# Kernel optimization log

Hardware: AMD Instinct MI355X
Metric: run time of the kernel (lower is better)

## Reference

```python
import jax, jax.numpy as jnp
import numpy as np

H, N, S, R, CH, LMAX = 512, 32, 1, 1, 1, 1024


def _to_c(x):
    # torch.view_as_real storage -> complex
    return x[..., 0] + 1j * x[..., 1]


def _rep(x, v):
    # einops: '... t n -> ... (v t) n'  (tile trainable copies up to H)
    shp = x.shape
    x = jnp.broadcast_to(x[..., None, :, :], shp[:-2] + (v,) + shp[-2:])
    return x.reshape(shp[:-2] + (v * shp[-2], shp[-1]))


def setup_inputs() -> dict:
    key = jax.random.key(0)
    k1, k2, k3, k4, k5 = jax.random.split(key, 5)
    # dt log-uniform in [1e-3, 1e-1] (S4 default init)
    log_dt = jax.random.uniform(k1, (H,), jnp.float32,
                                minval=float(np.log(1e-3)), maxval=float(np.log(1e-1)))
    # real_type='exp': w_real = -exp(inv_w_real); init around -0.5
    inv_w_real = jnp.log(0.5) * jnp.ones((S, N), jnp.float32) \
        + 0.1 * jax.random.normal(k2, (S, N), jnp.float32)
    w_imag = jnp.broadcast_to(jnp.pi * jnp.arange(N, dtype=jnp.float32), (S, N))
    B_ri = jax.random.normal(k3, (1, S, N, 2), jnp.float32)
    C_ri = jax.random.normal(k4, (CH, H, N, 2), jnp.float32)
    P_ri = 0.5 * jax.random.normal(k5, (R, S, N, 2), jnp.float32)
    return {"log_dt": log_dt, "inv_w_real": inv_w_real, "w_imag": w_imag,
            "B_ri": B_ri, "C_ri": C_ri, "P_ri": P_ri, "L": LMAX}


def _kernel(log_dt, inv_w_real, w_imag, B_ri, C_ri, P_ri, L):
    dt = jnp.exp(log_dt)                                    # (H,)
    w = -jnp.exp(inv_w_real) + 1j * w_imag                  # (S, N), real_type='exp'
    B = _to_c(B_ri)                                         # (1, S, N)
    C = _to_c(C_ri)                                         # (c, H, N)
    P = _to_c(P_ri)                                         # (R, S, N)
    Q = jnp.conj(P)
    v_rep = log_dt.shape[0] // w.shape[0]                   # broadcast = H // S
    B, P, Q = _rep(B, v_rep), _rep(P, v_rep), _rep(Q, v_rep)
    w = _rep(w, v_rep)                                      # (H, N)
    rank = P.shape[0]

    # FFT nodes and bilinear-transformed nodes
    Lf = L // 2 + 1
    omega = jnp.exp(-2j * jnp.pi * jnp.arange(Lf) / L).astype(jnp.complex64)
    z = 2 * (1 - omega) / (1 + omega)                       # (Lf,)

    # Stack B with P and C with Q for batched Cauchy
    Bst = jnp.concatenate([B, P], axis=-3)                  # (1+R, H, N)
    Cst = jnp.concatenate([C, Q], axis=-3)                  # (c+R, H, N)
    v = Bst[:, None] * Cst[None]                            # (1+R, c+R, H, N)
    w_dt = w * dt[:, None]                                  # (H, N): dt folded into A

    # Cauchy kernel with conjugate-pair extension: sum_n v/(z-w) + conj(v)/(z-conj(w))
    v2 = jnp.concatenate([v, jnp.conj(v)], axis=-1)         # (1+R, c+R, H, 2N)
    w2 = jnp.concatenate([w_dt, jnp.conj(w_dt)], axis=-1)   # (H, 2N)
    r = jnp.sum(v2[..., None] / (z - w2[..., :, None]), axis=-2)  # (1+R, c+R, H, Lf)
    r = r * dt[None, None, :, None]

    # Woodbury correction for the low-rank part
    r00 = r[:-rank, :-rank]                                 # (1, c, H, Lf)
    r01 = r[:-rank, -rank:]                                 # (1, R, H, Lf)
    r10 = r[-rank:, :-rank]                                 # (R, c, H, Lf)
    r11 = r[-rank:, -rank:]                                 # (R, R, H, Lf)
    r11 = jnp.moveaxis(r11, (0, 1), (-2, -1))               # (H, Lf, R, R)
    r11 = jnp.linalg.inv(jnp.eye(rank, dtype=r.dtype) + r11)
    r11 = jnp.moveaxis(r11, (-2, -1), (0, 1))               # (R, R, H, Lf)
    k_f = r00 - jnp.einsum('ijhl,jkhl,kmhl->imhl', r01, r11, r10)

    # Undo bilinear transform and go to time domain
    k_f = k_f * 2 / (1 + omega)
    k = jnp.fft.irfft(k_f, n=L, axis=-1)[..., :L]           # (1, c, H, L) real
    return k[-1]                                            # k_B: (c, H, L)


def reference(log_dt, inv_w_real, w_imag, B_ri, C_ri, P_ri, L):
    return _kernel(log_dt, inv_w_real, w_imag, B_ri, C_ri, P_ri, L)
```

## Files before the change

### kernel.cpp

```cpp
#include <hip/hip_runtime.h>
#include <math.h>

#define H_DIM 512
#define N_DIM 32
#define L_LEN 1024

typedef float v2f __attribute__((ext_vector_type(2)));
__device__ __forceinline__ v2f splat2(float a) { return (v2f){a, a}; }


__launch_bounds__(576, 5)
__global__ void ssk_nplr_kernel(const float* __restrict__ log_dt,
                                const float* __restrict__ inv_w_real,
                                const float* __restrict__ w_imag,
                                const float* __restrict__ B_ri,
                                const float* __restrict__ C_ri,
                                const float* __restrict__ P_ri,
                                float* __restrict__ out)
{
    __shared__ float2 Ksh[513];
    __shared__ float2 polD[N_DIM];
    __shared__ float4 polA[N_DIM];
    __shared__ float4 polB[N_DIM];
    __shared__ float  Sre[512], Sim[512];

    const int t = threadIdx.x;
    const int h = blockIdx.x;
    const float dt = expf(log_dt[h]);

    if (t < N_DIM) {
        const int n = t;
        float wr = -expf(inv_w_real[n]);
        float wi = w_imag[n];
        float wdx = wr * dt, wdy = wi * dt;
        float Bx = B_ri[2*n],               By = B_ri[2*n+1];
        float Cx = C_ri[h*2*N_DIM + 2*n],   Cy = C_ri[h*2*N_DIM + 2*n+1];
        float Px = P_ri[2*n],               Py = P_ri[2*n+1];
        float v00x = Bx*Cx - By*Cy, v00y = Bx*Cy + By*Cx;
        float v01x = Bx*Px + By*Py, v01y = By*Px - Bx*Py;
        float v10x = Px*Cx - Py*Cy, v10y = Px*Cy + Py*Cx;
        float v11x = Px*Px + Py*Py;
        polD[n] = make_float2(-2.0f*wdx, wdx*wdx + wdy*wdy);
        polA[n] = make_float4(2.0f*v00x, 2.0f*v01x, 2.0f*v10x, 2.0f*v11x);
        polB[n] = make_float4(2.0f*(v00x*wdx + v00y*wdy),
                              2.0f*(v01x*wdx + v01y*wdy),
                              2.0f*(v10x*wdx + v10y*wdy),
                              2.0f*(v11x*wdx));
    }

    float w256c, w256s, w128c, w128s, w64c, w64s;
    float w32c, w32s, w16c, w16s, w8c, w8s, w4c, w4s;
    {
        float r256 = (float)(t & 255) * (1.0f/512.0f);
        float r128 = (float)(t & 127) * (1.0f/256.0f);
        float r64  = (float)(t &  63) * (1.0f/128.0f);
        float r32  = (float)(t &  31) * (1.0f/64.0f);
        float r16  = (float)(t &  15) * (1.0f/32.0f);
        float r8   = (float)(t &   7) * (1.0f/16.0f);
        float r4   = (float)(t &   3) * (1.0f/8.0f);
        w256s = __builtin_amdgcn_sinf(r256); w256c = __builtin_amdgcn_cosf(r256);
        w128s = __builtin_amdgcn_sinf(r128); w128c = __builtin_amdgcn_cosf(r128);
        w64s  = __builtin_amdgcn_sinf(r64);  w64c  = __builtin_amdgcn_cosf(r64);
        w32s  = __builtin_amdgcn_sinf(r32);  w32c  = __builtin_amdgcn_cosf(r32);
        w16s  = __builtin_amdgcn_sinf(r16);  w16c  = __builtin_amdgcn_cosf(r16);
        w8s   = __builtin_amdgcn_sinf(r8);   w8c   = __builtin_amdgcn_cosf(r8);
        w4s   = __builtin_amdgcn_sinf(r4);   w4c   = __builtin_amdgcn_cosf(r4);
    }

    const int j = (t < 512) ? t : 512;
    float si, co;
    if (j == 512) {
        si = 8.7422777e-8f;
        co = -1.0f;
    } else {
        float rev = (float)j * (-0.0009765625f);
        si = __builtin_amdgcn_sinf(rev);
        co = __builtin_amdgcn_cosf(rev);
    }
    __syncthreads();

    float px = 1.0f + co, py = si;
    float pinv = 1.0f / (px*px + py*py);
    float ipx = px*pinv, ipy = -py*pinv;
    float mx = 1.0f - co, my = -si;
    float zx = 2.0f*(mx*ipx - my*ipy);
    float zy = 2.0f*(mx*ipy + my*ipx);

    v2f Z  = { zx, zy };
    v2f Z2 = { zx*zx - zy*zy, 2.0f*zx*zy };

    v2f U0{0,0}, U1{0,0}, U2{0,0}, U3{0,0};
    v2f V0{0,0}, V1{0,0}, V2{0,0}, V3{0,0};
    #pragma unroll 4
    for (int n = 0; n < N_DIM; ++n) {
        float2 d  = polD[n];
        float4 A  = polA[n];
        float4 Bv = polB[n];
        v2f D = __builtin_elementwise_fma(splat2(d.x), Z, Z2);
        D.x += d.y;
        float s  = __builtin_amdgcn_rcpf(fmaf(D.x, D.x, D.y*D.y));
        v2f R = { D.x * s, -(D.y * s) };
        U0 = __builtin_elementwise_fma(splat2(A.x),  R, U0);
        U1 = __builtin_elementwise_fma(splat2(A.y),  R, U1);
        U2 = __builtin_elementwise_fma(splat2(A.z),  R, U2);
        U3 = __builtin_elementwise_fma(splat2(A.w),  R, U3);
        V0 = __builtin_elementwise_fma(splat2(Bv.x), R, V0);
        V1 = __builtin_elementwise_fma(splat2(Bv.y), R, V1);
        V2 = __builtin_elementwise_fma(splat2(Bv.z), R, V2);
        V3 = __builtin_elementwise_fma(splat2(Bv.w), R, V3);
    }
    float r00x = dt*(zx*U0.x - zy*U0.y - V0.x), r00y = dt*(zx*U0.y + zy*U0.x - V0.y);
    float r01x = dt*(zx*U1.x - zy*U1.y - V1.x), r01y = dt*(zx*U1.y + zy*U1.x - V1.y);
    float r10x = dt*(zx*U2.x - zy*U2.y - V2.x), r10y = dt*(zx*U2.y + zy*U2.x - V2.y);
    float r11x = dt*(zx*U3.x - zy*U3.y - V3.x), r11y = dt*(zx*U3.y + zy*U3.x - V3.y);

    float dnx = 1.0f + r11x, dny = r11y;
    float dinv = 1.0f / (dnx*dnx + dny*dny);
    float idx_ = dnx*dinv, idy = -dny*dinv;
    float m01x = r01x*r10x - r01y*r10y;
    float m01y = r01x*r10y + r01y*r10x;
    float kfx = r00x - (m01x*idx_ - m01y*idy);
    float kfy = r00y - (m01x*idy + m01y*idx_);
    float fxv = 2.0f*(kfx*ipx - kfy*ipy);
    float fyv = 2.0f*(kfx*ipy + kfy*ipx);
    if (t <= 512) Ksh[j] = make_float2(fxv, fyv);
    __syncthreads();

    float xr = 0.0f, xi = 0.0f;
    if (t < 512) {
        float2 Ka = Ksh[t];
        float2 Kb = Ksh[512 - t];
        const int tb = t ^ 256;
        float2 Kc = Ksh[tb];
        float2 Kd = Ksh[512 - tb];
        float Wx = co, Wy = -si;
        float hsx = 0.5f*(Ka.x + Kb.x), hsy = 0.5f*(Ka.y - Kb.y);
        float hdx = 0.5f*(Ka.x - Kb.x), hdy = 0.5f*(Ka.y + Kb.y);
        float Yax = hsx - Wy*hdx - Wx*hdy;
        float Yay = hsy - Wy*hdy + Wx*hdx;
        float Wbx = (t < 256) ? -Wy :  Wy;
        float Wby = (t < 256) ?  Wx : -Wx;
        float hsx2 = 0.5f*(Kc.x + Kd.x), hsy2 = 0.5f*(Kc.y - Kd.y);
        float hdx2 = 0.5f*(Kc.x - Kd.x), hdy2 = 0.5f*(Kc.y + Kd.y);
        float Ybx = hsx2 - Wby*hdx2 - Wbx*hdy2;
        float Yby = hsy2 - Wby*hdy2 + Wbx*hdx2;
        if (t & 256) {
            float dr = Ybx - Yax, di = Yby - Yay;
            xr = dr*w256c - di*w256s; xi = dr*w256s + di*w256c;
        } else {
            xr = Yax + Ybx; xi = Yay + Yby;
        }
        Sre[t] = xr; Sim[t] = xi;
    }
    __syncthreads();

    if (t < 512) {
        {
            float p1r = Sre[t ^ 128], p1i = Sim[t ^ 128];
            float p2r = Sre[t ^  64], p2i = Sim[t ^  64];
            float p3r = Sre[t ^ 192], p3i = Sim[t ^ 192];
            float Atr, Ati, Apr, Api;
            if (t & 128) {
                float dr = p1r - xr, di = p1i - xi;
                Atr = dr*w128c - di*w128s; Ati = dr*w128s + di*w128c;
                float er = p3r - p2r, ei = p3i - p2i;
                float wpr = (t & 64) ?  w128s : -w128s;
                float wpi = (t & 64) ? -w128c :  w128c;
                Apr = er*wpr - ei*wpi; Api = er*wpi + ei*wpr;
            } else {
                Atr = xr + p1r;  Ati = xi + p1i;
                Apr = p2r + p3r; Api = p2i + p3i;
            }
            if (t & 64) {
                float dr = Apr - Atr, di = Api - Ati;
                xr = dr*w64c - di*w64s; xi = dr*w64s + di*w64c;
            } else { xr = Atr + Apr; xi = Ati + Api; }
        }

        #define RADIX4S(S_, W1C, W1S, W2C, W2S) {                               \
            float p1r = __shfl_xor(xr, S_),        p1i = __shfl_xor(xi, S_);    \
            float p2r = __shfl_xor(xr, S_/2),      p2i = __shfl_xor(xi, S_/2);  \
            float p3r = __shfl_xor(xr, S_ + S_/2), p3i = __shfl_xor(xi, S_ + S_/2); \
            float Atr, Ati, Apr, Api;                                           \
            if (t & S_) {                                                       \
                float dr = p1r - xr, di = p1i - xi;                             \
                Atr = dr*W1C - di*W1S; Ati = dr*W1S + di*W1C;                   \
                float er = p3r - p2r, ei = p3i - p2i;                           \
                float wpr = (t & (S_/2)) ?  W1S : -W1S;                         \
                float wpi = (t & (S_/2)) ? -W1C :  W1C;                         \
                Apr = er*wpr - ei*wpi; Api = er*wpi + ei*wpr;                   \
            } else {                                                            \
                Atr = xr + p1r;  Ati = xi + p1i;                                \
                Apr = p2r + p3r; Api = p2i + p3i;                               \
            }                                                                   \
            if (t & (S_/2)) {                                                   \
                float dr = Apr - Atr, di = Api - Ati;                           \
                xr = dr*W2C - di*W2S; xi = dr*W2S + di*W2C;                     \
            } else { xr = Atr + Apr; xi = Ati + Api; }                          \
        }
        RADIX4S(32, w32c, w32s, w16c, w16s)
        RADIX4S(8,  w8c,  w8s,  w4c,  w4s)
        #undef RADIX4S

        {
            float p1r = __shfl_xor(xr, 2), p1i = __shfl_xor(xi, 2);
            float p2r = __shfl_xor(xr, 1), p2i = __shfl_xor(xi, 1);
            float p3r = __shfl_xor(xr, 3), p3i = __shfl_xor(xi, 3);
            float Atr, Ati, Apr, Api;
            if (t & 2) {
                float dr = p1r - xr, di = p1i - xi;
                float er = p3r - p2r, ei = p3i - p2i;
                if (t & 1) { Atr = -di; Ati =  dr;
                             Apr =  er; Api =  ei; }
                else       { Atr =  dr; Ati =  di;
                             Apr = -ei; Api =  er; }
            } else {
                Atr = xr + p1r;  Ati = xi + p1i;
                Apr = p2r + p3r; Api = p2i + p3i;
            }
            if (t & 1) { xr = Apr - Atr; xi = Api - Ati; }
            else       { xr = Atr + Apr; xi = Ati + Api; }
        }

        unsigned m = __brev((unsigned)t) >> 23;
        ((float2*)out)[h*512 + m] = make_float2(xr*(1.0f/512.0f), xi*(1.0f/512.0f));
    }
}

extern "C" void kernel_launch(void* const* d_in, const int* in_sizes, int n_in,
                              void* d_out, int out_size, void* d_ws, size_t ws_size,
                              hipStream_t stream) {
    const float* log_dt     = (const float*)d_in[0];
    const float* inv_w_real = (const float*)d_in[1];
    const float* w_imag     = (const float*)d_in[2];
    const float* B_ri       = (const float*)d_in[3];
    const float* C_ri       = (const float*)d_in[4];
    const float* P_ri       = (const float*)d_in[5];

    ssk_nplr_kernel<<<H_DIM, 576, 0, stream>>>(log_dt, inv_w_real, w_imag,
                                               B_ri, C_ri, P_ri, (float*)d_out);
}
```

Before: 15.86 us.

## Split Cauchy evaluation and inverse FFT into two kernels with N-split reduction

Splits the fused kernel into a Cauchy kernel and an iFFT kernel that exchange the frequency response through a workspace buffer. The Cauchy kernel uses a 2D grid over frequency chunks, splits the 32-term sum across four thread groups and reduces their partials through shared memory. This is meant to raise parallelism and shorten each thread's serial loop. In exchange it adds a second launch, a global round trip for kf, and wastes most of the last frequency block (only j=512 is valid there).

```diff
diff --git a/kernel.cpp b/kernel.cpp
--- a/kernel.cpp
+++ b/kernel.cpp
@@ -4,28 +4,31 @@
 #define H_DIM 512
 #define N_DIM 32
 #define L_LEN 1024
+#define LF 513
 
 typedef float v2f __attribute__((ext_vector_type(2)));
-__device__ __forceinline__ v2f splat2(float a) { return (v2f){a, a}; }
-
-
-__launch_bounds__(576, 5)
-__global__ void ssk_nplr_kernel(const float* __restrict__ log_dt,
-                                const float* __restrict__ inv_w_real,
-                                const float* __restrict__ w_imag,
-                                const float* __restrict__ B_ri,
-                                const float* __restrict__ C_ri,
-                                const float* __restrict__ P_ri,
-                                float* __restrict__ out)
+static __device__ __forceinline__ v2f splat2(float a) { return (v2f){a, a}; }
+
+__launch_bounds__(512, 8)
+__global__ void k1_cauchy(const float* __restrict__ log_dt,
+                          const float* __restrict__ inv_w_real,
+                          const float* __restrict__ w_imag,
+                          const float* __restrict__ B_ri,
+                          const float* __restrict__ C_ri,
+                          const float* __restrict__ P_ri,
+                          float2* __restrict__ kf)
 {
-    __shared__ float2 Ksh[513];
     __shared__ float2 polD[N_DIM];
     __shared__ float4 polA[N_DIM];
     __shared__ float4 polB[N_DIM];
-    __shared__ float  Sre[512], Sim[512];
-
-    const int t = threadIdx.x;
-    const int h = blockIdx.x;
+    __shared__ float4 comb[4][4][128];
+
+    const int t  = threadIdx.x;
+    const int h  = blockIdx.x;
+    const int jl = t & 127;
+    const int ph = t >> 7;
+    const int j  = blockIdx.y * 128 + jl;
+    const bool active = (j <= 512);
     const float dt = expf(log_dt[h]);
 
     if (t < N_DIM) {
@@ -47,27 +50,8 @@
                               2.0f*(v10x*wdx + v10y*wdy),
                               2.0f*(v11x*wdx));
     }
-
-    float w256c, w256s, w128c, w128s, w64c, w64s;
-    float w32c, w32s, w16c, w16s, w8c, w8s, w4c, w4s;
-    {
-        float r256 = (float)(t & 255) * (1.0f/512.0f);
-        float r128 = (float)(t & 127) * (1.0f/256.0f);
-        float r64  = (float)(t &  63) * (1.0f/128.0f);
-        float r32  = (float)(t &  31) * (1.0f/64.0f);
-        float r16  = (float)(t &  15) * (1.0f/32.0f);
-        float r8   = (float)(t &   7) * (1.0f/16.0f);
-        float r4   = (float)(t &   3) * (1.0f/8.0f);
-        w256s = __builtin_amdgcn_sinf(r256); w256c = __builtin_amdgcn_cosf(r256);
-        w128s = __builtin_amdgcn_sinf(r128); w128c = __builtin_amdgcn_cosf(r128);
-        w64s  = __builtin_amdgcn_sinf(r64);  w64c  = __builtin_amdgcn_cosf(r64);
-        w32s  = __builtin_amdgcn_sinf(r32);  w32c  = __builtin_amdgcn_cosf(r32);
-        w16s  = __builtin_amdgcn_sinf(r16);  w16c  = __builtin_amdgcn_cosf(r16);
-        w8s   = __builtin_amdgcn_sinf(r8);   w8c   = __builtin_amdgcn_cosf(r8);
-        w4s   = __builtin_amdgcn_sinf(r4);   w4c   = __builtin_amdgcn_cosf(r4);
-    }
-
-    const int j = (t < 512) ? t : 512;
+    __syncthreads();
+
     float si, co;
     if (j == 512) {
         si = 8.7422777e-8f;
@@ -77,7 +61,6 @@
         si = __builtin_amdgcn_sinf(rev);
         co = __builtin_amdgcn_cosf(rev);
     }
-    __syncthreads();
 
     float px = 1.0f + co, py = si;
     float pinv = 1.0f / (px*px + py*py);
@@ -91,8 +74,10 @@
 
     v2f U0{0,0}, U1{0,0}, U2{0,0}, U3{0,0};
     v2f V0{0,0}, V1{0,0}, V2{0,0}, V3{0,0};
-    #pragma unroll 4
-    for (int n = 0; n < N_DIM; ++n) {
+    const int n0 = ph * 8;
+    #pragma unroll
+    for (int k = 0; k < 8; ++k) {
+        const int n = n0 + k;
         float2 d  = polD[n];
         float4 A  = polA[n];
         float4 Bv = polB[n];
@@ -109,25 +94,81 @@
         V2 = __builtin_elementwise_fma(splat2(Bv.z), R, V2);
         V3 = __builtin_elementwise_fma(splat2(Bv.w), R, V3);
     }
-    float r00x = dt*(zx*U0.x - zy*U0.y - V0.x), r00y = dt*(zx*U0.y + zy*U0.x - V0.y);
-    float r01x = dt*(zx*U1.x - zy*U1.y - V1.x), r01y = dt*(zx*U1.y + zy*U1.x - V1.y);
-    float r10x = dt*(zx*U2.x - zy*U2.y - V2.x), r10y = dt*(zx*U2.y + zy*U2.x - V2.y);
-    float r11x = dt*(zx*U3.x - zy*U3.y - V3.x), r11y = dt*(zx*U3.y + zy*U3.x - V3.y);
-
-    float dnx = 1.0f + r11x, dny = r11y;
-    float dinv = 1.0f / (dnx*dnx + dny*dny);
-    float idx_ = dnx*dinv, idy = -dny*dinv;
-    float m01x = r01x*r10x - r01y*r10y;
-    float m01y = r01x*r10y + r01y*r10x;
-    float kfx = r00x - (m01x*idx_ - m01y*idy);
-    float kfy = r00y - (m01x*idy + m01y*idx_);
-    float fxv = 2.0f*(kfx*ipx - kfy*ipy);
-    float fyv = 2.0f*(kfx*ipy + kfy*ipx);
-    if (t <= 512) Ksh[j] = make_float2(fxv, fyv);
-    __syncthreads();
-
-    float xr = 0.0f, xi = 0.0f;
-    if (t < 512) {
+
+    comb[ph][0][jl] = make_float4(U0.x, U0.y, U1.x, U1.y);
+    comb[ph][1][jl] = make_float4(U2.x, U2.y, U3.x, U3.y);
+    comb[ph][2][jl] = make_float4(V0.x, V0.y, V1.x, V1.y);
+    comb[ph][3][jl] = make_float4(V2.x, V2.y, V3.x, V3.y);
+    __syncthreads();
+
+    if (ph == 0 && active) {
+        #pragma unroll
+        for (int p = 1; p < 4; ++p) {
+            float4 c0 = comb[p][0][jl];
+            float4 c1 = comb[p][1][jl];
+            float4 c2 = comb[p][2][jl];
+            float4 c3 = comb[p][3][jl];
+            U0.x += c0.x; U0.y += c0.y; U1.x += c0.z; U1.y += c0.w;
+            U2.x += c1.x; U2.y += c1.y; U3.x += c1.z; U3.y += c1.w;
+            V0.x += c2.x; V0.y += c2.y; V1.x += c2.z; V1.y += c2.w;
+            V2.x += c3.x; V2.y += c3.y; V3.x += c3.z; V3.y += c3.w;
+        }
+        float r00x = dt*(zx*U0.x - zy*U0.y - V0.x), r00y = dt*(zx*U0.y + zy*U0.x - V0.y);
+        float r01x = dt*(zx*U1.x - zy*U1.y - V1.x), r01y = dt*(zx*U1.y + zy*U1.x - V1.y);
+        float r10x = dt*(zx*U2.x - zy*U2.y - V2.x), r10y = dt*(zx*U2.y + zy*U2.x - V2.y);
+        float r11x = dt*(zx*U3.x - zy*U3.y - V3.x), r11y = dt*(zx*U3.y + zy*U3.x - V3.y);
+
+        float dnx = 1.0f + r11x, dny = r11y;
+        float dinv = 1.0f / (dnx*dnx + dny*dny);
+        float idx_ = dnx*dinv, idy = -dny*dinv;
+        float m01x = r01x*r10x - r01y*r10y;
+        float m01y = r01x*r10y + r01y*r10x;
+        float kfx = r00x - (m01x*idx_ - m01y*idy);
+        float kfy = r00y - (m01x*idy + m01y*idx_);
+        float fxv = 2.0f*(kfx*ipx - kfy*ipy);
+        float fyv = 2.0f*(kfx*ipy + kfy*ipx);
+        kf[h*LF + j] = make_float2(fxv, fyv);
+    }
+}
+
+__launch_bounds__(512, 8)
+__global__ void k2_ifft(const float2* __restrict__ kf,
+                        float* __restrict__ out)
+{
+    __shared__ float2 Ksh[LF];
+    __shared__ float  Sre[512], Sim[512];
+
+    const int t = threadIdx.x;
+    const int h = blockIdx.x;
+
+    Ksh[t] = kf[h*LF + t];
+    if (t == 0) Ksh[512] = kf[h*LF + 512];
+
+    float w256c, w256s, w128c, w128s, w64c, w64s;
+    float w32c, w32s, w16c, w16s, w8c, w8s, w4c, w4s;
+    {
+        float r256 = (float)(t & 255) * (1.0f/512.0f);
+        float r128 = (float)(t & 127) * (1.0f/256.0f);
+        float r64  = (float)(t &  63) * (1.0f/128.0f);
+        float r32  = (float)(t &  31) * (1.0f/64.0f);
+        float r16  = (float)(t &  15) * (1.0f/32.0f);
+        float r8   = (float)(t &   7) * (1.0f/16.0f);
+        float r4   = (float)(t &   3) * (1.0f/8.0f);
+        w256s = __builtin_amdgcn_sinf(r256); w256c = __builtin_amdgcn_cosf(r256);
+        w128s = __builtin_amdgcn_sinf(r128); w128c = __builtin_amdgcn_cosf(r128);
+        w64s  = __builtin_amdgcn_sinf(r64);  w64c  = __builtin_amdgcn_cosf(r64);
+        w32s  = __builtin_amdgcn_sinf(r32);  w32c  = __builtin_amdgcn_cosf(r32);
+        w16s  = __builtin_amdgcn_sinf(r16);  w16c  = __builtin_amdgcn_cosf(r16);
+        w8s   = __builtin_amdgcn_sinf(r8);   w8c   = __builtin_amdgcn_cosf(r8);
+        w4s   = __builtin_amdgcn_sinf(r4);   w4c   = __builtin_amdgcn_cosf(r4);
+    }
+    float rev = (float)t * (-0.0009765625f);
+    float si = __builtin_amdgcn_sinf(rev);
+    float co = __builtin_amdgcn_cosf(rev);
+    __syncthreads();
+
+    float xr, xi;
+    {
         float2 Ka = Ksh[t];
         float2 Kb = Ksh[512 - t];
         const int tb = t ^ 256;
@@ -154,77 +195,75 @@
     }
     __syncthreads();
 
-    if (t < 512) {
-        {
-            float p1r = Sre[t ^ 128], p1i = Sim[t ^ 128];
-            float p2r = Sre[t ^  64], p2i = Sim[t ^  64];
-            float p3r = Sre[t ^ 192], p3i = Sim[t ^ 192];
-            float Atr, Ati, Apr, Api;
-            if (t & 128) {
-                float dr = p1r - xr, di = p1i - xi;
-                Atr = dr*w128c - di*w128s; Ati = dr*w128s + di*w128c;
-                float er = p3r - p2r, ei = p3i - p2i;
-                float wpr = (t & 64) ?  w128s : -w128s;
-                float wpi = (t & 64) ? -w128c :  w128c;
-                Apr = er*wpr - ei*wpi; Api = er*wpi + ei*wpr;
-            } else {
-                Atr = xr + p1r;  Ati = xi + p1i;
-                Apr = p2r + p3r; Api = p2i + p3i;
-            }
-            if (t & 64) {
-                float dr = Apr - Atr, di = Api - Ati;
-                xr = dr*w64c - di*w64s; xi = dr*w64s + di*w64c;
-            } else { xr = Atr + Apr; xi = Ati + Api; }
-        }
-
-        #define RADIX4S(S_, W1C, W1S, W2C, W2S) {                               \
-            float p1r = __shfl_xor(xr, S_),        p1i = __shfl_xor(xi, S_);    \
-            float p2r = __shfl_xor(xr, S_/2),      p2i = __shfl_xor(xi, S_/2);  \
-            float p3r = __shfl_xor(xr, S_ + S_/2), p3i = __shfl_xor(xi, S_ + S_/2); \
-            float Atr, Ati, Apr, Api;                                           \
-            if (t & S_) {                                                       \
-                float dr = p1r - xr, di = p1i - xi;                             \
-                Atr = dr*W1C - di*W1S; Ati = dr*W1S + di*W1C;                   \
-                float er = p3r - p2r, ei = p3i - p2i;                           \
-                float wpr = (t & (S_/2)) ?  W1S : -W1S;                         \
-                float wpi = (t & (S_/2)) ? -W1C :  W1C;                         \
-                Apr = er*wpr - ei*wpi; Api = er*wpi + ei*wpr;                   \
-            } else {                                                            \
-                Atr = xr + p1r;  Ati = xi + p1i;                                \
-                Apr = p2r + p3r; Api = p2i + p3i;                               \
-            }                                                                   \
-            if (t & (S_/2)) {                                                   \
-                float dr = Apr - Atr, di = Api - Ati;                           \
-                xr = dr*W2C - di*W2S; xi = dr*W2S + di*W2C;                     \
-            } else { xr = Atr + Apr; xi = Ati + Api; }                          \
-        }
-        RADIX4S(32, w32c, w32s, w16c, w16s)
-        RADIX4S(8,  w8c,  w8s,  w4c,  w4s)
-        #undef RADIX4S
-
-        {
-            float p1r = __shfl_xor(xr, 2), p1i = __shfl_xor(xi, 2);
-            float p2r = __shfl_xor(xr, 1), p2i = __shfl_xor(xi, 1);
-            float p3r = __shfl_xor(xr, 3), p3i = __shfl_xor(xi, 3);
-            float Atr, Ati, Apr, Api;
-            if (t & 2) {
-                float dr = p1r - xr, di = p1i - xi;
-                float er = p3r - p2r, ei = p3i - p2i;
-                if (t & 1) { Atr = -di; Ati =  dr;
-                             Apr =  er; Api =  ei; }
-                else       { Atr =  dr; Ati =  di;
-                             Apr = -ei; Api =  er; }
-            } else {
-                Atr = xr + p1r;  Ati = xi + p1i;
-                Apr = p2r + p3r; Api = p2i + p3i;
-            }
-            if (t & 1) { xr = Apr - Atr; xi = Api - Ati; }
-            else       { xr = Atr + Apr; xi = Ati + Api; }
-        }
-
-        unsigned m = __brev((unsigned)t) >> 23;
-        ((float2*)out)[h*512 + m] = make_float2(xr*(1.0f/512.0f), xi*(1.0f/512.0f));
-    }
+    {
+        float p1r = Sre[t ^ 128], p1i = Sim[t ^ 128];
+        float p2r = Sre[t ^  64], p2i = Sim[t ^  64];
+        float p3r = Sre[t ^ 192], p3i = Sim[t ^ 192];
+        float Atr, Ati, Apr, Api;
+        if (t & 128) {
+            float dr = p1r - xr, di = p1i - xi;
+            Atr = dr*w128c - di*w128s; Ati = dr*w128s + di*w128c;
+            float er = p3r - p2r, ei = p3i - p2i;
+            float wpr = (t & 64) ?  w128s : -w128s;
+            float wpi = (t & 64) ? -w128c :  w128c;
+            Apr = er*wpr - ei*wpi; Api = er*wpi + ei*wpr;
+        } else {
+            Atr = xr + p1r;  Ati = xi + p1i;
+            Apr = p2r + p3r; Api = p2i + p3i;
+        }
+        if (t & 64) {
+            float dr = Apr - Atr, di = Api - Ati;
+            xr = dr*w64c - di*w64s; xi = dr*w64s + di*w64c;
+        } else { xr = Atr + Apr; xi = Ati + Api; }
+    }
+
+    #define RADIX4S(S_, W1C, W1S, W2C, W2S) {                               \
+        float p1r = __shfl_xor(xr, S_),        p1i = __shfl_xor(xi, S_);    \
+        float p2r = __shfl_xor(xr, S_/2),      p2i = __shfl_xor(xi, S_/2);  \
+        float p3r = __shfl_xor(xr, S_ + S_/2), p3i = __shfl_xor(xi, S_ + S_/2); \
+        float Atr, Ati, Apr, Api;                                           \
+        if (t & S_) {                                                       \
+            float dr = p1r - xr, di = p1i - xi;                             \
+            Atr = dr*W1C - di*W1S; Ati = dr*W1S + di*W1C;                   \
+            float er = p3r - p2r, ei = p3i - p2i;                           \
+            float wpr = (t & (S_/2)) ?  W1S : -W1S;                         \
+            float wpi = (t & (S_/2)) ? -W1C :  W1C;                         \
+            Apr = er*wpr - ei*wpi; Api = er*wpi + ei*wpr;                   \
+        } else {                                                            \
+            Atr = xr + p1r;  Ati = xi + p1i;                                \
+            Apr = p2r + p3r; Api = p2i + p3i;                               \
+        }                                                                   \
+        if (t & (S_/2)) {                                                   \
+            float dr = Apr - Atr, di = Api - Ati;                           \
+            xr = dr*W2C - di*W2S; xi = dr*W2S + di*W2C;                     \
+        } else { xr = Atr + Apr; xi = Ati + Api; }                          \
+    }
+    RADIX4S(32, w32c, w32s, w16c, w16s)
+    RADIX4S(8,  w8c,  w8s,  w4c,  w4s)
+    #undef RADIX4S
+
+    {
+        float p1r = __shfl_xor(xr, 2), p1i = __shfl_xor(xi, 2);
+        float p2r = __shfl_xor(xr, 1), p2i = __shfl_xor(xi, 1);
+        float p3r = __shfl_xor(xr, 3), p3i = __shfl_xor(xi, 3);
+        float Atr, Ati, Apr, Api;
+        if (t & 2) {
+            float dr = p1r - xr, di = p1i - xi;
+            float er = p3r - p2r, ei = p3i - p2i;
+            if (t & 1) { Atr = -di; Ati =  dr;
+                         Apr =  er; Api =  ei; }
+            else       { Atr =  dr; Ati =  di;
+                         Apr = -ei; Api =  er; }
+        } else {
+            Atr = xr + p1r;  Ati = xi + p1i;
+            Apr = p2r + p3r; Api = p2i + p3i;
+        }
+        if (t & 1) { xr = Apr - Atr; xi = Api - Ati; }
+        else       { xr = Atr + Apr; xi = Ati + Api; }
+    }
+
+    unsigned m = __brev((unsigned)t) >> 23;
+    ((float2*)out)[h*512 + m] = make_float2(xr*(1.0f/512.0f), xi*(1.0f/512.0f));
 }
 
 extern "C" void kernel_launch(void* const* d_in, const int* in_sizes, int n_in,
@@ -237,6 +276,10 @@
     const float* C_ri       = (const float*)d_in[4];
     const float* P_ri       = (const float*)d_in[5];
 
-    ssk_nplr_kernel<<<H_DIM, 576, 0, stream>>>(log_dt, inv_w_real, w_imag,
-                                               B_ri, C_ri, P_ri, (float*)d_out);
+    float2* kf = (float2*)d_ws;
+
+    dim3 g1(H_DIM, 5);
+    k1_cauchy<<<g1, 512, 0, stream>>>(log_dt, inv_w_real, w_imag,
+                                      B_ri, C_ri, P_ri, kf);
+    k2_ifft<<<H_DIM, 512, 0, stream>>>(kf, (float*)d_out);
 }
```

Result: slower. 19.35 us (+22.0%).

## Compute two frequency nodes per thread in Cauchy stage, shrink block to 512

Applied to the files above, without the earlier changes.

Block size drops from 576 to 512 threads. In the Cauchy/Woodbury stage, threads 0..256 now each evaluate two frequency nodes (j and j+256), so the shared-memory loads of the pole coefficients are reused across both nodes and the partial wavefront of 64 extra threads goes away. The FFT stage keeps one point per thread and its twiddle is computed separately. In exchange, about half the threads sit idle during the Cauchy loop, and register pressure rises from the doubled accumulators.

```diff
diff --git a/kernel.cpp b/kernel.cpp
--- a/kernel.cpp
+++ b/kernel.cpp
@@ -3,13 +3,31 @@
 
 #define H_DIM 512
 #define N_DIM 32
-#define L_LEN 1024
 
 typedef float v2f __attribute__((ext_vector_type(2)));
-__device__ __forceinline__ v2f splat2(float a) { return (v2f){a, a}; }
-
-
-__launch_bounds__(576, 5)
+static __device__ __forceinline__ v2f splat2(float a) { return (v2f){a, a}; }
+
+static __device__ __forceinline__ float2 woodbury(
+    v2f U0, v2f U1, v2f U2, v2f U3,
+    v2f V0, v2f V1, v2f V2, v2f V3,
+    float zx, float zy, float dt, float ipx, float ipy)
+{
+    float r00x = dt*(zx*U0.x - zy*U0.y - V0.x), r00y = dt*(zx*U0.y + zy*U0.x - V0.y);
+    float r01x = dt*(zx*U1.x - zy*U1.y - V1.x), r01y = dt*(zx*U1.y + zy*U1.x - V1.y);
+    float r10x = dt*(zx*U2.x - zy*U2.y - V2.x), r10y = dt*(zx*U2.y + zy*U2.x - V2.y);
+    float r11x = dt*(zx*U3.x - zy*U3.y - V3.x), r11y = dt*(zx*U3.y + zy*U3.x - V3.y);
+    float dnx = 1.0f + r11x, dny = r11y;
+    float dinv = 1.0f / (dnx*dnx + dny*dny);
+    float idx_ = dnx*dinv, idy = -dny*dinv;
+    float m01x = r01x*r10x - r01y*r10y;
+    float m01y = r01x*r10y + r01y*r10x;
+    float kfx = r00x - (m01x*idx_ - m01y*idy);
+    float kfy = r00y - (m01x*idy + m01y*idx_);
+    return make_float2(2.0f*(kfx*ipx - kfy*ipy),
+                       2.0f*(kfx*ipy + kfy*ipx));
+}
+
+__launch_bounds__(512, 4)
 __global__ void ssk_nplr_kernel(const float* __restrict__ log_dt,
                                 const float* __restrict__ inv_w_real,
                                 const float* __restrict__ w_imag,
@@ -66,74 +84,100 @@
         w8s   = __builtin_amdgcn_sinf(r8);   w8c   = __builtin_amdgcn_cosf(r8);
         w4s   = __builtin_amdgcn_sinf(r4);   w4c   = __builtin_amdgcn_cosf(r4);
     }
-
-    const int j = (t < 512) ? t : 512;
-    float si, co;
-    if (j == 512) {
-        si = 8.7422777e-8f;
-        co = -1.0f;
-    } else {
-        float rev = (float)j * (-0.0009765625f);
-        si = __builtin_amdgcn_sinf(rev);
-        co = __builtin_amdgcn_cosf(rev);
+    float Wx, Wy;
+    {
+        float pr = (float)t * 0.0009765625f;
+        Wy = __builtin_amdgcn_sinf(pr);
+        Wx = __builtin_amdgcn_cosf(pr);
     }
     __syncthreads();
 
-    float px = 1.0f + co, py = si;
-    float pinv = 1.0f / (px*px + py*py);
-    float ipx = px*pinv, ipy = -py*pinv;
-    float mx = 1.0f - co, my = -si;
-    float zx = 2.0f*(mx*ipx - my*ipy);
-    float zy = 2.0f*(mx*ipy + my*ipx);
-
-    v2f Z  = { zx, zy };
-    v2f Z2 = { zx*zx - zy*zy, 2.0f*zx*zy };
-
-    v2f U0{0,0}, U1{0,0}, U2{0,0}, U3{0,0};
-    v2f V0{0,0}, V1{0,0}, V2{0,0}, V3{0,0};
-    #pragma unroll 4
-    for (int n = 0; n < N_DIM; ++n) {
-        float2 d  = polD[n];
-        float4 A  = polA[n];
-        float4 Bv = polB[n];
-        v2f D = __builtin_elementwise_fma(splat2(d.x), Z, Z2);
-        D.x += d.y;
-        float s  = __builtin_amdgcn_rcpf(fmaf(D.x, D.x, D.y*D.y));
-        v2f R = { D.x * s, -(D.y * s) };
-        U0 = __builtin_elementwise_fma(splat2(A.x),  R, U0);
-        U1 = __builtin_elementwise_fma(splat2(A.y),  R, U1);
-        U2 = __builtin_elementwise_fma(splat2(A.z),  R, U2);
-        U3 = __builtin_elementwise_fma(splat2(A.w),  R, U3);
-        V0 = __builtin_elementwise_fma(splat2(Bv.x), R, V0);
-        V1 = __builtin_elementwise_fma(splat2(Bv.y), R, V1);
-        V2 = __builtin_elementwise_fma(splat2(Bv.z), R, V2);
-        V3 = __builtin_elementwise_fma(splat2(Bv.w), R, V3);
-    }
-    float r00x = dt*(zx*U0.x - zy*U0.y - V0.x), r00y = dt*(zx*U0.y + zy*U0.x - V0.y);
-    float r01x = dt*(zx*U1.x - zy*U1.y - V1.x), r01y = dt*(zx*U1.y + zy*U1.x - V1.y);
-    float r10x = dt*(zx*U2.x - zy*U2.y - V2.x), r10y = dt*(zx*U2.y + zy*U2.x - V2.y);
-    float r11x = dt*(zx*U3.x - zy*U3.y - V3.x), r11y = dt*(zx*U3.y + zy*U3.x - V3.y);
-
-    float dnx = 1.0f + r11x, dny = r11y;
-    float dinv = 1.0f / (dnx*dnx + dny*dny);
-    float idx_ = dnx*dinv, idy = -dny*dinv;
-    float m01x = r01x*r10x - r01y*r10y;
-    float m01y = r01x*r10y + r01y*r10x;
-    float kfx = r00x - (m01x*idx_ - m01y*idy);
-    float kfy = r00y - (m01x*idy + m01y*idx_);
-    float fxv = 2.0f*(kfx*ipx - kfy*ipy);
-    float fyv = 2.0f*(kfx*ipy + kfy*ipx);
-    if (t <= 512) Ksh[j] = make_float2(fxv, fyv);
+    if (t < 257) {
+        const int j1 = t, j2 = t + 256;
+        float s1, c1, s2, c2;
+        {
+            float rev1 = (float)j1 * (-0.0009765625f);
+            s1 = __builtin_amdgcn_sinf(rev1);
+            c1 = __builtin_amdgcn_cosf(rev1);
+        }
+        if (j2 == 512) {
+            s2 = 8.7422777e-8f;
+            c2 = -1.0f;
+        } else {
+            float rev2 = (float)j2 * (-0.0009765625f);
+            s2 = __builtin_amdgcn_sinf(rev2);
+            c2 = __builtin_amdgcn_cosf(rev2);
+        }
+
+        float pxa = 1.0f + c1, pya = s1;
+        float pia = 1.0f / (pxa*pxa + pya*pya);
+        float ipxa = pxa*pia, ipya = -pya*pia;
+        float mxa = 1.0f - c1, mya = -s1;
+        float zxa = 2.0f*(mxa*ipxa - mya*ipya);
+        float zya = 2.0f*(mxa*ipya + mya*ipxa);
+
+        float pxb = 1.0f + c2, pyb = s2;
+        float pib = 1.0f / (pxb*pxb + pyb*pyb);
+        float ipxb = pxb*pib, ipyb = -pyb*pib;
+        float mxb = 1.0f - c2, myb = -s2;
+        float zxb = 2.0f*(mxb*ipxb - myb*ipyb);
+        float zyb = 2.0f*(mxb*ipyb + myb*ipxb);
+
+        v2f Za  = { zxa, zya };
+        v2f Z2a = { zxa*zxa - zya*zya, 2.0f*zxa*zya };
+        v2f Zb  = { zxb, zyb };
+        v2f Z2b = { zxb*zxb - zyb*zyb, 2.0f*zxb*zyb };
+
+        v2f Ua0{0,0}, Ua1{0,0}, Ua2{0,0}, Ua3{0,0};
+        v2f Va0{0,0}, Va1{0,0}, Va2{0,0}, Va3{0,0};
+        v2f Ub0{0,0}, Ub1{0,0}, Ub2{0,0}, Ub3{0,0};
+        v2f Vb0{0,0}, Vb1{0,0}, Vb2{0,0}, Vb3{0,0};
+
+        #pragma unroll 4
+        for (int n = 0; n < N_DIM; ++n) {
+            float2 d  = polD[n];
+            float4 A  = polA[n];
+            float4 Bv = polB[n];
+            v2f Da = __builtin_elementwise_fma(splat2(d.x), Za, Z2a);
+            Da.x += d.y;
+            v2f Db = __builtin_elementwise_fma(splat2(d.x), Zb, Z2b);
+            Db.x += d.y;
+            float sa = __builtin_amdgcn_rcpf(fmaf(Da.x, Da.x, Da.y*Da.y));
+            float sb = __builtin_amdgcn_rcpf(fmaf(Db.x, Db.x, Db.y*Db.y));
+            v2f Ra = { Da.x * sa, -(Da.y * sa) };
+            v2f Rb = { Db.x * sb, -(Db.y * sb) };
+            Ua0 = __builtin_elementwise_fma(splat2(A.x),  Ra, Ua0);
+            Ua1 = __builtin_elementwise_fma(splat2(A.y),  Ra, Ua1);
+            Ua2 = __builtin_elementwise_fma(splat2(A.z),  Ra, Ua2);
+            Ua3 = __builtin_elementwise_fma(splat2(A.w),  Ra, Ua3);
+            Va0 = __builtin_elementwise_fma(splat2(Bv.x), Ra, Va0);
+            Va1 = __builtin_elementwise_fma(splat2(Bv.y), Ra, Va1);
+            Va2 = __builtin_elementwise_fma(splat2(Bv.z), Ra, Va2);
+            Va3 = __builtin_elementwise_fma(splat2(Bv.w), Ra, Va3);
+            Ub0 = __builtin_elementwise_fma(splat2(A.x),  Rb, Ub0);
+            Ub1 = __builtin_elementwise_fma(splat2(A.y),  Rb, Ub1);
+            Ub2 = __builtin_elementwise_fma(splat2(A.z),  Rb, Ub2);
+            Ub3 = __builtin_elementwise_fma(splat2(A.w),  Rb, Ub3);
+            Vb0 = __builtin_elementwise_fma(splat2(Bv.x), Rb, Vb0);
+            Vb1 = __builtin_elementwise_fma(splat2(Bv.y), Rb, Vb1);
+            Vb2 = __builtin_elementwise_fma(splat2(Bv.z), Rb, Vb2);
+            Vb3 = __builtin_elementwise_fma(splat2(Bv.w), Rb, Vb3);
+        }
+
+        Ksh[j1] = woodbury(Ua0, Ua1, Ua2, Ua3, Va0, Va1, Va2, Va3,
+                           zxa, zya, dt, ipxa, ipya);
+        Ksh[j2] = woodbury(Ub0, Ub1, Ub2, Ub3, Vb0, Vb1, Vb2, Vb3,
+                           zxb, zyb, dt, ipxb, ipyb);
+    }
     __syncthreads();
 
-    float xr = 0.0f, xi = 0.0f;
-    if (t < 512) {
+    float xr, xi;
+    {
         float2 Ka = Ksh[t];
         float2 Kb = Ksh[512 - t];
         const int tb = t ^ 256;
         float2 Kc = Ksh[tb];
         float2 Kd = Ksh[512 - tb];
-        float Wx = co, Wy = -si;
         float hsx = 0.5f*(Ka.x + Kb.x), hsy = 0.5f*(Ka.y - Kb.y);
         float hdx = 0.5f*(Ka.x - Kb.x), hdy = 0.5f*(Ka.y + Kb.y);
         float Yax = hsx - Wy*hdx - Wx*hdy;
@@ -154,77 +198,75 @@
     }
     __syncthreads();
 
-    if (t < 512) {
-        {
-            float p1r = Sre[t ^ 128], p1i = Sim[t ^ 128];
-            float p2r = Sre[t ^  64], p2i = Sim[t ^  64];
-            float p3r = Sre[t ^ 192], p3i = Sim[t ^ 192];
-            float Atr, Ati, Apr, Api;
-            if (t & 128) {
-                float dr = p1r - xr, di = p1i - xi;
-                Atr = dr*w128c - di*w128s; Ati = dr*w128s + di*w128c;
-                float er = p3r - p2r, ei = p3i - p2i;
-                float wpr = (t & 64) ?  w128s : -w128s;
-                float wpi = (t & 64) ? -w128c :  w128c;
-                Apr = er*wpr - ei*wpi; Api = er*wpi + ei*wpr;
-            } else {
-                Atr = xr + p1r;  Ati = xi + p1i;
-                Apr = p2r + p3r; Api = p2i + p3i;
-            }
-            if (t & 64) {
-                float dr = Apr - Atr, di = Api - Ati;
-                xr = dr*w64c - di*w64s; xi = dr*w64s + di*w64c;
-            } else { xr = Atr + Apr; xi = Ati + Api; }
-        }
-
-        #define RADIX4S(S_, W1C, W1S, W2C, W2S) {                               \
-            float p1r = __shfl_xor(xr, S_),        p1i = __shfl_xor(xi, S_);    \
-            float p2r = __shfl_xor(xr, S_/2),      p2i = __shfl_xor(xi, S_/2);  \
-            float p3r = __shfl_xor(xr, S_ + S_/2), p3i = __shfl_xor(xi, S_ + S_/2); \
-            float Atr, Ati, Apr, Api;                                           \
-            if (t & S_) {                                                       \
-                float dr = p1r - xr, di = p1i - xi;                             \
-                Atr = dr*W1C - di*W1S; Ati = dr*W1S + di*W1C;                   \
-                float er = p3r - p2r, ei = p3i - p2i;                           \
-                float wpr = (t & (S_/2)) ?  W1S : -W1S;                         \
-                float wpi = (t & (S_/2)) ? -W1C :  W1C;                         \
-                Apr = er*wpr - ei*wpi; Api = er*wpi + ei*wpr;                   \
-            } else {                                                            \
-                Atr = xr + p1r;  Ati = xi + p1i;                                \
-                Apr = p2r + p3r; Api = p2i + p3i;                               \
-            }                                                                   \
-            if (t & (S_/2)) {                                                   \
-                float dr = Apr - Atr, di = Api - Ati;                           \
-                xr = dr*W2C - di*W2S; xi = dr*W2S + di*W2C;                     \
-            } else { xr = Atr + Apr; xi = Ati + Api; }                          \
-        }
-        RADIX4S(32, w32c, w32s, w16c, w16s)
-        RADIX4S(8,  w8c,  w8s,  w4c,  w4s)
-        #undef RADIX4S
-
-        {
-            float p1r = __shfl_xor(xr, 2), p1i = __shfl_xor(xi, 2);
-            float p2r = __shfl_xor(xr, 1), p2i = __shfl_xor(xi, 1);
-            float p3r = __shfl_xor(xr, 3), p3i = __shfl_xor(xi, 3);
-            float Atr, Ati, Apr, Api;
-            if (t & 2) {
-                float dr = p1r - xr, di = p1i - xi;
-                float er = p3r - p2r, ei = p3i - p2i;
-                if (t & 1) { Atr = -di; Ati =  dr;
-                             Apr =  er; Api =  ei; }
-                else       { Atr =  dr; Ati =  di;
-                             Apr = -ei; Api =  er; }
-            } else {
-                Atr = xr + p1r;  Ati = xi + p1i;
-                Apr = p2r + p3r; Api = p2i + p3i;
-            }
-            if (t & 1) { xr = Apr - Atr; xi = Api - Ati; }
-            else       { xr = Atr + Apr; xi = Ati + Api; }
-        }
-
-        unsigned m = __brev((unsigned)t) >> 23;
-        ((float2*)out)[h*512 + m] = make_float2(xr*(1.0f/512.0f), xi*(1.0f/512.0f));
-    }
+    {
+        float p1r = Sre[t ^ 128], p1i = Sim[t ^ 128];
+        float p2r = Sre[t ^  64], p2i = Sim[t ^  64];
+        float p3r = Sre[t ^ 192], p3i = Sim[t ^ 192];
+        float Atr, Ati, Apr, Api;
+        if (t & 128) {
+            float dr = p1r - xr, di = p1i - xi;
+            Atr = dr*w128c - di*w128s; Ati = dr*w128s + di*w128c;
+            float er = p3r - p2r, ei = p3i - p2i;
+            float wpr = (t & 64) ?  w128s : -w128s;
+            float wpi = (t & 64) ? -w128c :  w128c;
+            Apr = er*wpr - ei*wpi; Api = er*wpi + ei*wpr;
+        } else {
+            Atr = xr + p1r;  Ati = xi + p1i;
+            Apr = p2r + p3r; Api = p2i + p3i;
+        }
+        if (t & 64) {
+            float dr = Apr - Atr, di = Api - Ati;
+            xr = dr*w64c - di*w64s; xi = dr*w64s + di*w64c;
+        } else { xr = Atr + Apr; xi = Ati + Api; }
+    }
+
+    #define RADIX4S(S_, W1C, W1S, W2C, W2S) {                               \
+        float p1r = __shfl_xor(xr, S_),        p1i = __shfl_xor(xi, S_);    \
+        float p2r = __shfl_xor(xr, S_/2),      p2i = __shfl_xor(xi, S_/2);  \
+        float p3r = __shfl_xor(xr, S_ + S_/2), p3i = __shfl_xor(xi, S_ + S_/2); \
+        float Atr, Ati, Apr, Api;                                           \
+        if (t & S_) {                                                       \
+            float dr = p1r - xr, di = p1i - xi;                             \
+            Atr = dr*W1C - di*W1S; Ati = dr*W1S + di*W1C;                   \
+            float er = p3r - p2r, ei = p3i - p2i;                           \
+            float wpr = (t & (S_/2)) ?  W1S : -W1S;                         \
+            float wpi = (t & (S_/2)) ? -W1C :  W1C;                         \
+            Apr = er*wpr - ei*wpi; Api = er*wpi + ei*wpr;                   \
+        } else {                                                            \
+            Atr = xr + p1r;  Ati = xi + p1i;                                \
+            Apr = p2r + p3r; Api = p2i + p3i;                               \
+        }                                                                   \
+        if (t & (S_/2)) {                                                   \
+            float dr = Apr - Atr, di = Api - Ati;                           \
+            xr = dr*W2C - di*W2S; xi = dr*W2S + di*W2C;                     \
+        } else { xr = Atr + Apr; xi = Ati + Api; }                          \
+    }
+    RADIX4S(32, w32c, w32s, w16c, w16s)
+    RADIX4S(8,  w8c,  w8s,  w4c,  w4s)
+    #undef RADIX4S
+
+    {
+        float p1r = __shfl_xor(xr, 2), p1i = __shfl_xor(xi, 2);
+        float p2r = __shfl_xor(xr, 1), p2i = __shfl_xor(xi, 1);
+        float p3r = __shfl_xor(xr, 3), p3i = __shfl_xor(xi, 3);
+        float Atr, Ati, Apr, Api;
+        if (t & 2) {
+            float dr = p1r - xr, di = p1i - xi;
+            float er = p3r - p2r, ei = p3i - p2i;
+            if (t & 1) { Atr = -di; Ati =  dr;
+                         Apr =  er; Api =  ei; }
+            else       { Atr =  dr; Ati =  di;
+                         Apr = -ei; Api =  er; }
+        } else {
+            Atr = xr + p1r;  Ati = xi + p1i;
+            Apr = p2r + p3r; Api = p2i + p3i;
+        }
+        if (t & 1) { xr = Apr - Atr; xi = Api - Ati; }
+        else       { xr = Atr + Apr; xi = Ati + Api; }
+    }
+
+    unsigned m = __brev((unsigned)t) >> 23;
+    ((float2*)out)[h*512 + m] = make_float2(xr*(1.0f/512.0f), xi*(1.0f/512.0f));
 }
 
 extern "C" void kernel_launch(void* const* d_in, const int* in_sizes, int n_in,
@@ -237,6 +279,6 @@
     const float* C_ri       = (const float*)d_in[4];
     const float* P_ri       = (const float*)d_in[5];
 
-    ssk_nplr_kernel<<<H_DIM, 576, 0, stream>>>(log_dt, inv_w_real, w_imag,
+    ssk_nplr_kernel<<<H_DIM, 512, 0, stream>>>(log_dt, inv_w_real, w_imag,
                                                B_ri, C_ri, P_ri, (float*)d_out);
 }
```

Result: slower. 16.43 us (+3.6%).
